# Optimization experiments

Measured on AMD Instinct MI355X. Metric: run time of the kernel, lower is better.

## Reference

```python
import jax, jax.numpy as jnp
import numpy as np

N = 1024          # number of proposals
D_APP = 1024      # appearance_feature_dim
D_K = 64          # key_feature_dim
D_G = 64          # geo_feature_dim
NR = 16           # n_relations


def setup_inputs() -> dict:
    key = jax.random.key(0)
    ks = jax.random.split(key, 12)
    s = 0.02
    return {
        "f_a": jax.random.normal(ks[0], (N, D_APP), dtype=jnp.float32),
        "position_embedding": jax.random.uniform(ks[1], (N, N, D_G), dtype=jnp.float32),
        # stacked per-relation params; torch Linear weight layout [out, in]
        "WG_w": jax.random.normal(ks[2], (NR, D_G), dtype=jnp.float32) * s,
        "WG_b": jax.random.normal(ks[3], (NR,), dtype=jnp.float32) * s,
        "WK_w": jax.random.normal(ks[4], (NR, D_K, D_APP), dtype=jnp.float32) * s,
        "WK_b": jax.random.normal(ks[5], (NR, D_K), dtype=jnp.float32) * s,
        "WQ_w": jax.random.normal(ks[6], (NR, D_K, D_APP), dtype=jnp.float32) * s,
        "WQ_b": jax.random.normal(ks[7], (NR, D_K), dtype=jnp.float32) * s,
        "WV_w": jax.random.normal(ks[8], (NR, D_K, D_APP), dtype=jnp.float32) * s,
        "WV_b": jax.random.normal(ks[9], (NR, D_K), dtype=jnp.float32) * s,
    }


def reference(f_a, position_embedding, WG_w, WG_b, WK_w, WK_b, WQ_w, WQ_b, WV_w, WV_b):
    n = f_a.shape[0]
    # geometric gate: relu(Linear(pos_emb)) per relation -> [R, N, N]
    pe = position_embedding.reshape(-1, WG_w.shape[1])  # [N*N, D_G]
    w_g = jax.nn.relu(jnp.einsum('pg,rg->rp', pe, WG_w) + WG_b[:, None])
    w_g = w_g.reshape(WG_w.shape[0], n, n)
    # per-relation K/Q/V projections: [R, N, D_K]
    K = jnp.einsum('nf,rdf->rnd', f_a, WK_w) + WK_b[:, None, :]
    Q = jnp.einsum('nf,rdf->rnd', f_a, WQ_w) + WQ_b[:, None, :]
    V = jnp.einsum('nf,rdf->rnd', f_a, WV_w) + WV_b[:, None, :]
    dk = K.shape[-1]
    # note: row index n comes from K, column index m from Q (as in the torch code)
    scores = jnp.einsum('rnd,rmd->rnm', K, Q) / jnp.sqrt(jnp.asarray(dk, K.dtype))
    w_mn = jnp.log(jnp.clip(w_g, 1e-6)) + scores
    attn = jax.nn.softmax(w_mn, axis=2)  # softmax over m (dim=1 in torch NxN view)
    out = jnp.einsum('rnm,rmd->rnd', attn, V)  # [R, N, D_K]
    R, _, d = out.shape
    concat = jnp.transpose(out, (1, 0, 2)).reshape(n, R * d)  # [N, R*D_K]
    return concat + f_a
```

## Files before the change

kernel.cpp:

```cpp
#include <hip/hip_runtime.h>
#include <hip/hip_bf16.h>
#include <hip/hip_fp16.h>
#include <math.h>

#define NN 1024
#define DAPP 1024
#define DK 64
#define DG 64
#define NR 16

typedef __bf16 bf16x8 __attribute__((ext_vector_type(8)));
typedef _Float16 f16x8 __attribute__((ext_vector_type(8)));
typedef _Float16 f16x4 __attribute__((ext_vector_type(4)));
typedef float f32x4 __attribute__((ext_vector_type(4)));

static constexpr size_t OFF_FAB = 0;
static constexpr size_t OFF_WB  = OFF_FAB + (size_t)NN * DAPP * 2;
static constexpr size_t OFF_KB  = OFF_WB + (size_t)3 * NR * DK * DAPP * 2;
static constexpr size_t OFF_QB  = OFF_KB + (size_t)NR * NN * DK * 2;
static constexpr size_t OFF_V   = OFF_QB + (size_t)NR * NN * DK * 2;
static constexpr size_t OFF_S   = OFF_V + (size_t)NR * NN * DK * 4;
static constexpr size_t OFF_ST  = OFF_S + (size_t)NR * NN * NN * 2;

__global__ __launch_bounds__(256) void cast_kernel(
    const float* __restrict__ fa, const float* __restrict__ wk,
    const float* __restrict__ wq, const float* __restrict__ wv,
    __bf16* __restrict__ fab, __bf16* __restrict__ wb) {
  int i = blockIdx.x * 256 + threadIdx.x;
  const int M1 = NN * DAPP;
  if (i < M1) {
    fab[i] = (__bf16)fa[i];
  } else {
    int j = i - M1;
    int p = j >> 20;
    int o = j & (M1 - 1);
    const float* src = (p == 0) ? wk : ((p == 1) ? wq : wv);
    wb[j] = (__bf16)src[o];
  }
}

__global__ __launch_bounds__(256) void kqv_kernel(
    const __bf16* __restrict__ fab, const __bf16* __restrict__ wb,
    const float* __restrict__ kbias, const float* __restrict__ qbias,
    const float* __restrict__ vbias,
    __bf16* __restrict__ Kb, __bf16* __restrict__ Qb, float* __restrict__ V) {
  int wave = blockIdx.x * 4 + (threadIdx.x >> 6);
  int l = threadIdx.x & 63;
  int nt = wave / 96;
  int jt = wave % 96;
  int n0 = nt * 32, j0 = jt * 32;
  int ra = l & 15;
  int ko = (l >> 4) * 8;

  f32x4 acc[2][2] = {};
  for (int k0 = 0; k0 < DAPP; k0 += 32) {
    bf16x8 a0 = *(const bf16x8*)(fab + (size_t)(n0 + ra) * DAPP + k0 + ko);
    bf16x8 a1 = *(const bf16x8*)(fab + (size_t)(n0 + 16 + ra) * DAPP + k0 + ko);
    bf16x8 b0 = *(const bf16x8*)(wb + (size_t)(j0 + ra) * DAPP + k0 + ko);
    bf16x8 b1 = *(const bf16x8*)(wb + (size_t)(j0 + 16 + ra) * DAPP + k0 + ko);
    acc[0][0] = __builtin_amdgcn_mfma_f32_16x16x32_bf16(a0, b0, acc[0][0], 0, 0, 0);
    acc[0][1] = __builtin_amdgcn_mfma_f32_16x16x32_bf16(a0, b1, acc[0][1], 0, 0, 0);
    acc[1][0] = __builtin_amdgcn_mfma_f32_16x16x32_bf16(a1, b0, acc[1][0], 0, 0, 0);
    acc[1][1] = __builtin_amdgcn_mfma_f32_16x16x32_bf16(a1, b1, acc[1][1], 0, 0, 0);
  }

  #pragma unroll
  for (int i = 0; i < 2; i++) {
    #pragma unroll
    for (int jj = 0; jj < 2; jj++) {
      #pragma unroll
      for (int q = 0; q < 4; q++) {
        int n = n0 + i * 16 + (l >> 4) * 4 + q;
        int col = j0 + jj * 16 + (l & 15);
        int proj = col >> 10;
        int rd = col & 1023;
        int r = rd >> 6, d = rd & 63;
        float v = acc[i][jj][q];
        size_t oidx = ((size_t)r * NN + n) * DK + d;
        if (proj == 0)      Kb[oidx] = (__bf16)(v + kbias[rd]);
        else if (proj == 1) Qb[oidx] = (__bf16)(v + qbias[rd]);
        else                V[oidx] = v + vbias[rd];
      }
    }
  }
}

__global__ __launch_bounds__(256) void gate_score_kernel(
    const float* __restrict__ pe, const float* __restrict__ WGw,
    const float* __restrict__ WGb,
    const __bf16* __restrict__ Kb, const __bf16* __restrict__ Qb,
    _Float16* __restrict__ X) {
  __shared__ float4 wgt[16][16];
  __shared__ float wgb[16];
  __shared__ _Float16 lg[16][16][36];
  int t = threadIdx.x;
  int nt = blockIdx.x >> 5, mc = blockIdx.x & 31;
  int n0 = nt * 16, m0 = mc * 32;
  {
    int g4 = t >> 4, r = t & 15;
    wgt[g4][r] = ((const float4*)WGw)[r * 16 + g4];
    if (t < 16) wgb[t] = WGb[t];
  }
  int l = t & 63, w = t >> 6;
  int rb = w * 4;
  int ra = l & 15;
  int ko = (l >> 4) * 8;

  bf16x8 kf[4][2];
  #pragma unroll
  for (int rr = 0; rr < 4; rr++)
    #pragma unroll
    for (int kk = 0; kk < 2; kk++)
      kf[rr][kk] = *(const bf16x8*)(Kb + (((size_t)(rb + rr) << 10) + n0 + ra) * DK + kk * 32 + ko);
  __syncthreads();

  #pragma unroll
  for (int pp = 0; pp < 2; pp++) {
    int p = t + pp * 256;
    int n = p >> 5, ml = p & 31;
    const float4* pe4 = (const float4*)(pe + (((size_t)(n0 + n) << 10) + m0 + ml) * DG);
    float acc[16];
    #pragma unroll
    for (int r = 0; r < 16; r++) acc[r] = wgb[r];
    #pragma unroll
    for (int g4 = 0; g4 < 16; g4++) {
      float4 pv = pe4[g4];
      #pragma unroll
      for (int r = 0; r < 16; r++) {
        float4 wv = wgt[g4][r];
        acc[r] = fmaf(pv.x, wv.x, fmaf(pv.y, wv.y, fmaf(pv.z, wv.z, fmaf(pv.w, wv.w, acc[r]))));
      }
    }
    #pragma unroll
    for (int r = 0; r < 16; r++)
      lg[r][n][ml] = (_Float16)__logf(fmaxf(acc[r], 1e-6f));
  }
  __syncthreads();

  #pragma unroll
  for (int rr = 0; rr < 4; rr++) {
    int r = rb + rr;
    const __bf16* Qr = Qb + (((size_t)r << 10)) * DK;
    #pragma unroll
    for (int mt = 0; mt < 2; mt++) {
      int mbase = m0 + mt * 16;
      f32x4 acc2 = {};
      #pragma unroll
      for (int kk = 0; kk < 2; kk++) {
        bf16x8 qa = *(const bf16x8*)(Qr + (size_t)(mbase + ra) * DK + kk * 32 + ko);
        acc2 = __builtin_amdgcn_mfma_f32_16x16x32_bf16(qa, kf[rr][kk], acc2, 0, 0, 0);
      }
      f16x4 lgv = *(const f16x4*)&lg[r][ra][mt * 16 + ((l >> 4) << 2)];
      f16x4 xv;
      #pragma unroll
      for (int q = 0; q < 4; q++)
        xv[q] = (_Float16)(acc2[q] * 0.125f + (float)lgv[q]);
      *(f16x4*)(X + ((size_t)r << 20) + ((size_t)(n0 + ra) << 10) + mbase + ((l >> 4) << 2)) = xv;
    }
  }
}

__global__ __launch_bounds__(256) void stats_kernel(
    const _Float16* __restrict__ X, float2* __restrict__ stats) {
  int row = blockIdx.x * 4 + (threadIdx.x >> 6);
  int l = threadIdx.x & 63;
  const f16x8* Sp = (const f16x8*)(X + ((size_t)row << 10) + l * 16);
  f16x8 a = Sp[0], b = Sp[1];
  float v[16];
  float mx = -1e30f;
  #pragma unroll
  for (int i = 0; i < 8; i++) { v[i] = (float)a[i]; v[8 + i] = (float)b[i]; }
  #pragma unroll
  for (int i = 0; i < 16; i++) mx = fmaxf(mx, v[i]);
  #pragma unroll
  for (int off = 32; off >= 1; off >>= 1) mx = fmaxf(mx, __shfl_xor(mx, off, 64));
  float sm = 0.f;
  #pragma unroll
  for (int i = 0; i < 16; i++) sm += __expf(v[i] - mx);
  #pragma unroll
  for (int off = 32; off >= 1; off >>= 1) sm += __shfl_xor(sm, off, 64);
  if (l == 0) stats[row] = make_float2(mx, sm);
}

__global__ __launch_bounds__(256) void pv_kernel(
    const _Float16* __restrict__ S, const float2* __restrict__ stats,
    const float* __restrict__ V, const float* __restrict__ fa,
    float* __restrict__ out) {
  int r = blockIdx.x >> 5;
  int n0 = (blockIdx.x & 31) * 32;
  __shared__ float Pt[64][36];
  __shared__ float Vt[64][68];
  __shared__ float2 st[32];
  int t = threadIdx.x;
  if (t < 32) st[t] = stats[r * NN + n0 + t];

  int d0 = (t & 15) * 4;
  int nl0 = (t >> 4) * 2;
  float acc[2][4] = {};

  for (int m0 = 0; m0 < NN; m0 += 64) {
    __syncthreads();
    {
      int nl = t >> 3;
      int ml = (t & 7) * 8;
      const _Float16* sp = S + ((size_t)r << 20) + ((size_t)(n0 + nl) << 10) + m0 + ml;
      f16x8 sv = *(const f16x8*)sp;
      float mxn = st[nl].x;
      #pragma unroll
      for (int u = 0; u < 8; u++) Pt[ml + u][nl] = __expf((float)sv[u] - mxn);
    }
    {
      int ml = t >> 2;
      int dq = (t & 3) * 16;
      const float* vp = V + ((size_t)r * NN + m0 + ml) * DK + dq;
      #pragma unroll
      for (int u = 0; u < 4; u++) {
        float4 vv = ((const float4*)vp)[u];
        *(float4*)&Vt[ml][dq + u * 4] = vv;
      }
    }
    __syncthreads();
    #pragma unroll 8
    for (int ml = 0; ml < 64; ml++) {
      float a0 = Pt[ml][nl0];
      float a1 = Pt[ml][nl0 + 1];
      float4 vv = *(const float4*)&Vt[ml][d0];
      acc[0][0] += a0 * vv.x; acc[0][1] += a0 * vv.y;
      acc[0][2] += a0 * vv.z; acc[0][3] += a0 * vv.w;
      acc[1][0] += a1 * vv.x; acc[1][1] += a1 * vv.y;
      acc[1][2] += a1 * vv.z; acc[1][3] += a1 * vv.w;
    }
  }

  #pragma unroll
  for (int i = 0; i < 2; i++) {
    int n = n0 + nl0 + i;
    float rs = 1.0f / st[nl0 + i].y;
    int col = r * DK + d0;
    const float4 f = *(const float4*)(fa + (size_t)n * DAPP + col);
    float4 o;
    o.x = acc[i][0] * rs + f.x;
    o.y = acc[i][1] * rs + f.y;
    o.z = acc[i][2] * rs + f.z;
    o.w = acc[i][3] * rs + f.w;
    *(float4*)(out + (size_t)n * DAPP + col) = o;
  }
}

extern "C" void kernel_launch(void* const* d_in, const int* in_sizes, int n_in,
                              void* d_out, int out_size, void* d_ws, size_t ws_size,
                              hipStream_t stream) {
  const float* fa  = (const float*)d_in[0];
  const float* pe  = (const float*)d_in[1];
  const float* WGw = (const float*)d_in[2];
  const float* WGb = (const float*)d_in[3];
  const float* WKw = (const float*)d_in[4];
  const float* WKb = (const float*)d_in[5];
  const float* WQw = (const float*)d_in[6];
  const float* WQb = (const float*)d_in[7];
  const float* WVw = (const float*)d_in[8];
  const float* WVb = (const float*)d_in[9];
  float* out = (float*)d_out;

  char* ws = (char*)d_ws;
  __bf16* fab = (__bf16*)(ws + OFF_FAB);
  __bf16* wb  = (__bf16*)(ws + OFF_WB);
  __bf16* Kb  = (__bf16*)(ws + OFF_KB);
  __bf16* Qb  = (__bf16*)(ws + OFF_QB);
  float*  V   = (float*)(ws + OFF_V);
  _Float16* X = (_Float16*)(ws + OFF_S);
  float2* st  = (float2*)(ws + OFF_ST);

  cast_kernel<<<16384, 256, 0, stream>>>(fa, WKw, WQw, WVw, fab, wb);
  kqv_kernel<<<768, 256, 0, stream>>>(fab, wb, WKb, WQb, WVb, Kb, Qb, V);
  gate_score_kernel<<<2048, 256, 0, stream>>>(pe, WGw, WGb, Kb, Qb, X);
  stats_kernel<<<4096, 256, 0, stream>>>(X, st);
  pv_kernel<<<512, 256, 0, stream>>>(X, st, V, fa, out);
}
```

Measured before the change: 568.7 us.

## Compute geometric gate projection with bf16 MFMA per wave-owned 16x16 tile

```diff
diff --git a/kernel.cpp b/kernel.cpp
--- a/kernel.cpp
+++ b/kernel.cpp
@@ -90,73 +90,66 @@
     const float* __restrict__ WGb,
     const __bf16* __restrict__ Kb, const __bf16* __restrict__ Qb,
     _Float16* __restrict__ X) {
-  __shared__ float4 wgt[16][16];
-  __shared__ float wgb[16];
-  __shared__ _Float16 lg[16][16][36];
+  __shared__ alignas(16) _Float16 lg[4][16][17][20];
   int t = threadIdx.x;
-  int nt = blockIdx.x >> 5, mc = blockIdx.x & 31;
-  int n0 = nt * 16, m0 = mc * 32;
-  {
-    int g4 = t >> 4, r = t & 15;
-    wgt[g4][r] = ((const float4*)WGw)[r * 16 + g4];
-    if (t < 16) wgb[t] = WGb[t];
-  }
   int l = t & 63, w = t >> 6;
-  int rb = w * 4;
-  int ra = l & 15;
-  int ko = (l >> 4) * 8;
-
-  bf16x8 kf[4][2];
-  #pragma unroll
-  for (int rr = 0; rr < 4; rr++)
-    #pragma unroll
-    for (int kk = 0; kk < 2; kk++)
-      kf[rr][kk] = *(const bf16x8*)(Kb + (((size_t)(rb + rr) << 10) + n0 + ra) * DK + kk * 32 + ko);
-  __syncthreads();
-
-  #pragma unroll
-  for (int pp = 0; pp < 2; pp++) {
-    int p = t + pp * 256;
-    int n = p >> 5, ml = p & 31;
-    const float4* pe4 = (const float4*)(pe + (((size_t)(n0 + n) << 10) + m0 + ml) * DG);
-    float acc[16];
-    #pragma unroll
-    for (int r = 0; r < 16; r++) acc[r] = wgb[r];
-    #pragma unroll
-    for (int g4 = 0; g4 < 16; g4++) {
-      float4 pv = pe4[g4];
-      #pragma unroll
-      for (int r = 0; r < 16; r++) {
-        float4 wv = wgt[g4][r];
-        acc[r] = fmaf(pv.x, wv.x, fmaf(pv.y, wv.y, fmaf(pv.z, wv.z, fmaf(pv.w, wv.w, acc[r]))));
-      }
-    }
-    #pragma unroll
-    for (int r = 0; r < 16; r++)
-      lg[r][n][ml] = (_Float16)__logf(fmaxf(acc[r], 1e-6f));
-  }
-  __syncthreads();
-
-  #pragma unroll
-  for (int rr = 0; rr < 4; rr++) {
-    int r = rb + rr;
+  int job = blockIdx.x * 4 + w;
+  int nt = job >> 6, mt = job & 63;
+  int n0 = nt * 16, m0 = mt * 16;
+  int pr = l & 15;
+  int kg = (l >> 4) * 8;
+  int mq = (l >> 4) << 2;
+
+  bf16x8 wgf[2];
+  #pragma unroll
+  for (int f = 0; f < 2; f++) {
+    const float* wp = WGw + pr * DG + f * 32 + kg;
+    float4 a = *(const float4*)wp;
+    float4 b = *(const float4*)(wp + 4);
+    bf16x8 v;
+    v[0] = (__bf16)a.x; v[1] = (__bf16)a.y; v[2] = (__bf16)a.z; v[3] = (__bf16)a.w;
+    v[4] = (__bf16)b.x; v[5] = (__bf16)b.y; v[6] = (__bf16)b.z; v[7] = (__bf16)b.w;
+    wgf[f] = v;
+  }
+  float biasr = WGb[pr];
+
+  #pragma unroll 4
+  for (int nl = 0; nl < 16; nl++) {
+    const float* pp = pe + (((size_t)(n0 + nl) << 10) + m0 + pr) * DG + kg;
+    f32x4 acc = {};
+    #pragma unroll
+    for (int f = 0; f < 2; f++) {
+      float4 a = *(const float4*)(pp + f * 32);
+      float4 b = *(const float4*)(pp + f * 32 + 4);
+      bf16x8 av;
+      av[0] = (__bf16)a.x; av[1] = (__bf16)a.y; av[2] = (__bf16)a.z; av[3] = (__bf16)a.w;
+      av[4] = (__bf16)b.x; av[5] = (__bf16)b.y; av[6] = (__bf16)b.z; av[7] = (__bf16)b.w;
+      acc = __builtin_amdgcn_mfma_f32_16x16x32_bf16(av, wgf[f], acc, 0, 0, 0);
+    }
+    f16x4 ov;
+    #pragma unroll
+    for (int q = 0; q < 4; q++)
+      ov[q] = (_Float16)__logf(fmaxf(acc[q] + biasr, 1e-6f));
+    *(f16x4*)&lg[w][pr][nl][mq] = ov;
+  }
+
+  #pragma unroll 4
+  for (int r = 0; r < 16; r++) {
+    const __bf16* Kr = Kb + (((size_t)r << 10)) * DK;
     const __bf16* Qr = Qb + (((size_t)r << 10)) * DK;
-    #pragma unroll
-    for (int mt = 0; mt < 2; mt++) {
-      int mbase = m0 + mt * 16;
-      f32x4 acc2 = {};
-      #pragma unroll
-      for (int kk = 0; kk < 2; kk++) {
-        bf16x8 qa = *(const bf16x8*)(Qr + (size_t)(mbase + ra) * DK + kk * 32 + ko);
-        acc2 = __builtin_amdgcn_mfma_f32_16x16x32_bf16(qa, kf[rr][kk], acc2, 0, 0, 0);
-      }
-      f16x4 lgv = *(const f16x4*)&lg[r][ra][mt * 16 + ((l >> 4) << 2)];
-      f16x4 xv;
-      #pragma unroll
-      for (int q = 0; q < 4; q++)
-        xv[q] = (_Float16)(acc2[q] * 0.125f + (float)lgv[q]);
-      *(f16x4*)(X + ((size_t)r << 20) + ((size_t)(n0 + ra) << 10) + mbase + ((l >> 4) << 2)) = xv;
-    }
+    f32x4 acc = {};
+    #pragma unroll
+    for (int f = 0; f < 2; f++) {
+      bf16x8 qa = *(const bf16x8*)(Qr + (size_t)(m0 + pr) * DK + f * 32 + kg);
+      bf16x8 kb = *(const bf16x8*)(Kr + (size_t)(n0 + pr) * DK + f * 32 + kg);
+      acc = __builtin_amdgcn_mfma_f32_16x16x32_bf16(qa, kb, acc, 0, 0, 0);
+    }
+    f16x4 lgv = *(const f16x4*)&lg[w][r][pr][mq];
+    f16x4 xv;
+    #pragma unroll
+    for (int q = 0; q < 4; q++)
+      xv[q] = (_Float16)(acc[q] * 0.125f + (float)lgv[q]);
+    *(f16x4*)(X + ((size_t)r << 20) + ((size_t)(n0 + pr) << 10) + m0 + mq) = xv;
   }
 }
 
@@ -273,7 +266,7 @@
 
   cast_kernel<<<16384, 256, 0, stream>>>(fa, WKw, WQw, WVw, fab, wb);
   kqv_kernel<<<768, 256, 0, stream>>>(fab, wb, WKb, WQb, WVb, Kb, Qb, V);
-  gate_score_kernel<<<2048, 256, 0, stream>>>(pe, WGw, WGb, Kb, Qb, X);
+  gate_score_kernel<<<1024, 256, 0, stream>>>(pe, WGw, WGb, Kb, Qb, X);
   stats_kernel<<<4096, 256, 0, stream>>>(X, st);
   pv_kernel<<<512, 256, 0, stream>>>(X, st, V, fa, out);
 }
```

Result: faster. 518.0 us (-8.9%).
